# Kernel tuning notes

Hardware: AMD Instinct MI355X
Metric: run time of the kernel (lower is better)

The kernel has to match this reference:

```python
import jax, jax.numpy as jnp
import numpy as np

TEMP = 0.07
MAX_SAMPLES = 2048
RADIUS = 10
HARD_FRAC = 0.75
FG_LABEL = 1
B, C, H, W = 8, 64, 256, 256
BLOCK = 32

MAX_FG = MAX_SAMPLES // 2                      # 1024
NEG_BUDGET = MAX_SAMPLES - MAX_FG              # 1024
HARD_BUDGET = int(round(HARD_FRAC * NEG_BUDGET))  # 768
RAND_BUDGET = NEG_BUDGET - HARD_BUDGET         # 256


def setup_inputs() -> dict:
    key = jax.random.key(0)
    feats = jax.random.normal(key, (B, C, H, W), dtype=jnp.float32)
    # 32x32-block checkerboard labels: guarantees abundant fg / ring / interior-bg pools
    ii, jj = jnp.meshgrid(jnp.arange(H), jnp.arange(W), indexing='ij')
    lbl = (((ii // BLOCK) + (jj // BLOCK)) % 2).astype(jnp.int32)
    labels = jnp.broadcast_to(lbl, (B, H, W))
    return {"feats": feats, "labels": labels}


def _forward(feats, labels):
    Bn, Cn, Hn, Wn = feats.shape
    n_pix = Hn * Wn
    f_flat = feats.reshape(Bn, Cn, n_pix).transpose(0, 2, 1)  # [B, P, C]
    l_flat = labels.reshape(Bn, n_pix)

    fg = labels == FG_LABEL                                   # [B, H, W]
    k = 2 * RADIUS + 1
    # max-pool dilation of fg mask (kernel k, stride 1, pad RADIUS == SAME)
    dil = jax.lax.reduce_window(fg.astype(jnp.float32), -jnp.inf, jax.lax.max,
                                (1, k, k), (1, 1, 1), 'SAME') > 0.0
    fg_flat = fg.reshape(Bn, n_pix)
    bg_flat = ~fg_flat                                        # all pixels valid (no ignore)
    ring_flat = dil.reshape(Bn, n_pix) & ~fg_flat & bg_flat
    bgonly_flat = bg_flat & ~ring_flat

    def per_image(f, y, fgm, ringm, bgm, key):
        k1, k2, k3 = jax.random.split(key, 3)
        def pick(mask, kk, n):
            # random subset of n true positions (== randperm[:n] in distribution)
            s = jnp.where(mask, jax.random.uniform(kk, mask.shape), -1.0)
            return jax.lax.top_k(s, n)[1]
        idx = jnp.concatenate([pick(fgm, k1, MAX_FG),
                               pick(ringm, k2, HARD_BUDGET),
                               pick(bgm, k3, RAND_BUDGET)])    # [K]
        fs = f[idx]                                            # [K, C]
        ys = y[idx]
        fs = fs / jnp.maximum(jnp.linalg.norm(fs, axis=1, keepdims=True), 1e-12)
        logits = fs @ fs.T / TEMP                              # [K, K]
        logits = logits - jax.lax.stop_gradient(logits.max(axis=1, keepdims=True))
        eye = jnp.eye(MAX_SAMPLES, dtype=bool)
        pos = (ys[:, None] == ys[None, :]) & ~eye
        exp_l = jnp.exp(logits) * (~eye)
        denom = jnp.maximum(exp_l.sum(axis=1), 1e-8)
        pos_sum = jnp.maximum(jnp.where(pos, exp_l, 0.0).sum(axis=1), 1e-8)
        valid = pos.any(axis=1) & (ys == FG_LABEL)
        loss_terms = -jnp.log(pos_sum / denom)
        n_valid = jnp.maximum(valid.sum(), 1)
        return jnp.where(valid, loss_terms, 0.0).sum() / n_valid

    keys = jax.random.split(jax.random.key(1), Bn)
    losses = jax.vmap(per_image)(f_flat, l_flat, fg_flat, ring_flat, bgonly_flat, keys)
    return losses.mean()


def reference(feats, labels):
    return _forward(feats, labels)
```

## Files before the change

kernel.cpp:

```cpp
#include <hip/hip_runtime.h>
#include <stdint.h>

#define NPIX   65536
#define NIMG   8
#define NCH    64
#define KSEL   2048
#define NFG    1024
#define NRING  768
#define NBG    256
#define INV_TEMP 14.285714285714286f

__device__ __forceinline__ void tf2x32(uint32_t k0, uint32_t k1,
                                       uint32_t& x0, uint32_t& x1) {
  const uint32_t ks2 = k0 ^ k1 ^ 0x1BD11BDAu;
  x0 += k0; x1 += k1;
#define TF_RND(r) { x0 += x1; x1 = (x1 << (r)) | (x1 >> (32 - (r))); x1 ^= x0; }
  TF_RND(13) TF_RND(15) TF_RND(26) TF_RND(6)
  x0 += k1;  x1 += ks2 + 1u;
  TF_RND(17) TF_RND(29) TF_RND(16) TF_RND(24)
  x0 += ks2; x1 += k0 + 2u;
  TF_RND(13) TF_RND(15) TF_RND(26) TF_RND(6)
  x0 += k0;  x1 += k1 + 3u;
  TF_RND(17) TF_RND(29) TF_RND(16) TF_RND(24)
  x0 += k1;  x1 += ks2 + 4u;
  TF_RND(13) TF_RND(15) TF_RND(26) TF_RND(6)
  x0 += ks2; x1 += k0 + 5u;
#undef TF_RND
}

#define ZERO_F4 1552
__global__ __launch_bounds__(1024) void dilate_pack(const int* __restrict__ labels,
                                                    uint64_t* __restrict__ fgw,
                                                    uint64_t* __restrict__ dilw,
                                                    float4* __restrict__ zregion,
                                                    uint32_t* __restrict__ keys,
                                                    float* __restrict__ out) {
  __shared__ uint64_t fgs[336], hds[336];
  const int tid = threadIdx.x;
  const int img = blockIdx.x >> 2;
  const int r0 = (blockIdx.x & 3) * 64;

  if (blockIdx.x == 0) {
    for (int t = tid; t < ZERO_F4; t += 1024)
      zregion[t] = make_float4(0.f, 0.f, 0.f, 0.f);
  } else if (blockIdx.x == 1 && tid == 0) {
    out[0] = 0.0f;
    for (int b = 0; b < NIMG; ++b) {
      uint32_t kb0 = 0u, kb1 = (uint32_t)b;
      tf2x32(0u, 1u, kb0, kb1);
      for (int g = 0; g < 3; ++g) {
        uint32_t x0 = 0u, x1 = (uint32_t)g;
        tf2x32(kb0, kb1, x0, x1);
        keys[(b * 3 + g) * 2 + 0] = x0;
        keys[(b * 3 + g) * 2 + 1] = x1;
      }
    }
  }

  #pragma unroll
  for (int it = 0; it < 21; ++it) {
    int li = it * 1024 + tid;
    int hr = r0 - 10 + (li >> 8);
    int col = li & 255;
    bool bit = false;
    if (hr >= 0 && hr < 256) bit = (labels[(img << 16) + (hr << 8) + col] == 1);
    uint64_t m = __ballot(bit);
    if ((tid & 63) == 0) fgs[li >> 6] = m;
  }
  __syncthreads();

  for (int w = tid; w < 336; w += 1024) {
    int wc = w & 3;
    uint64_t x = fgs[w];
    uint64_t L = wc > 0 ? fgs[w - 1] : 0ull;
    uint64_t R = wc < 3 ? fgs[w + 1] : 0ull;
    uint64_t acc = x;
    #pragma unroll
    for (int s = 1; s <= 10; ++s) {
      acc |= (x << s) | (L >> (64 - s));
      acc |= (x >> s) | (R << (64 - s));
    }
    hds[w] = acc;
  }
  __syncthreads();

  for (int w = tid; w < 256; w += 1024) {
    int r = w >> 2, wc = w & 3;
    int gr = r0 + r;
    uint64_t acc = 0ull;
    #pragma unroll
    for (int dr = 0; dr <= 20; ++dr) acc |= hds[(r + dr) * 4 + wc];
    fgw[img * 1024 + gr * 4 + wc]  = fgs[(r + 10) * 4 + wc];
    dilw[img * 1024 + gr * 4 + wc] = acc;
  }
}

__global__ __launch_bounds__(256) void hash_hist(const uint64_t* __restrict__ fgw,
                                                 const uint64_t* __restrict__ dilw,
                                                 const uint32_t* __restrict__ keys,
                                                 uint32_t* __restrict__ mgrp,
                                                 uint32_t* __restrict__ hist) {
  __shared__ uint32_t lh[768];
  __shared__ uint64_t fgl[32], dll[32];
  const int tid = threadIdx.x;
  for (int t = tid; t < 768; t += 256) lh[t] = 0;
  const int b = blockIdx.x >> 5;
  const int base = blockIdx.x * 2048;
  const int w0 = (blockIdx.x & 31) * 32;
  if (tid < 32) fgl[tid] = fgw[b * 1024 + w0 + tid];
  else if (tid < 64) dll[tid - 32] = dilw[b * 1024 + w0 + tid - 32];
  const uint32_t K00 = keys[b * 6 + 0], K01 = keys[b * 6 + 1];
  const uint32_t K10 = keys[b * 6 + 2], K11 = keys[b * 6 + 3];
  const uint32_t K20 = keys[b * 6 + 4], K21 = keys[b * 6 + 5];
  __syncthreads();

  #pragma unroll
  for (int k = 0; k < 8; ++k) {
    int off = k * 256 + tid;
    int pix = (base + off) & 65535;
    int lw = off >> 6, bp = off & 63;
    uint32_t fgbit = (uint32_t)((fgl[lw] >> bp) & 1ull);
    uint32_t dilbit = (uint32_t)((dll[lw] >> bp) & 1ull);
    uint32_t grp = fgbit ? 0u : (dilbit ? 1u : 2u);
    uint32_t k0 = grp == 0 ? K00 : grp == 1 ? K10 : K20;
    uint32_t k1 = grp == 0 ? K01 : grp == 1 ? K11 : K21;
    uint32_t x0 = 0u, x1 = (uint32_t)pix;
    tf2x32(k0, k1, x0, x1);
    uint32_t m = (x0 ^ x1) >> 9;
    mgrp[base + off] = (m << 2) | grp;
    atomicAdd(&lh[grp * 256 + (m >> 15)], 1u);
  }
  __syncthreads();
  for (int t = tid; t < 768; t += 256)
    if (lh[t]) atomicAdd(&hist[b * 768 + t], lh[t]);
}

__global__ __launch_bounds__(256) void topk_emit(const uint32_t* __restrict__ mgrp,
                                                 const uint32_t* __restrict__ hist,
                                                 uint32_t* __restrict__ TG,
                                                 uint32_t* __restrict__ cnt,
                                                 uint32_t* __restrict__ candcnt,
                                                 unsigned long long* __restrict__ cand,
                                                 int* __restrict__ idx_out) {
  __shared__ uint32_t hh[768];
  __shared__ uint32_t sT[3], loc[3], lbd[3], basA[3], basB[3];
  const int tid = threadIdx.x;
  const int b = blockIdx.x >> 5;
  const int base = blockIdx.x * 2048;
  for (int t = tid; t < 768; t += 256) hh[t] = hist[b * 768 + t];
  if (tid < 3) { loc[tid] = 0; lbd[tid] = 0; }
  __syncthreads();

  if (tid < 3) {
    uint32_t nsel = tid == 0 ? NFG : tid == 1 ? NRING : NBG;
    const uint32_t* h = hh + tid * 256;
    uint32_t cum = 0; int T = 255;
    for (; T > 0; --T) {
      uint32_t c = h[T];
      if (cum + c >= nsel) break;
      cum += c;
    }
    sT[tid] = (uint32_t)T;
    if ((blockIdx.x & 31) == 0) {
      TG[(b * 3 + tid) * 2] = (uint32_t)T;
      TG[(b * 3 + tid) * 2 + 1] = cum;
    }
  }
  __syncthreads();
  const uint32_t T0 = sT[0], T1 = sT[1], T2 = sT[2];

  #pragma unroll
  for (int k = 0; k < 8; ++k) {
    uint32_t v = mgrp[base + k * 256 + tid];
    uint32_t g = v & 3u, bin = v >> 17;
    uint32_t T = g == 0 ? T0 : g == 1 ? T1 : T2;
    if (bin > T) atomicAdd(&loc[g], 1u);
    else if (bin == T) atomicAdd(&lbd[g], 1u);
  }
  __syncthreads();
  if (tid < 3) {
    basA[tid] = atomicAdd(&cnt[b * 3 + tid], loc[tid]);
    basB[tid] = atomicAdd(&candcnt[b * 3 + tid], lbd[tid]);
    loc[tid] = 0; lbd[tid] = 0;
  }
  __syncthreads();

  #pragma unroll
  for (int k = 0; k < 8; ++k) {
    int p = base + k * 256 + tid;
    uint32_t v = mgrp[p];
    uint32_t g = v & 3u, bin = v >> 17;
    uint32_t T = g == 0 ? T0 : g == 1 ? T1 : T2;
    int pix = p & 65535;
    if (bin > T) {
      uint32_t o = atomicAdd(&loc[g], 1u);
      int seg = g == 0 ? 0 : g == 1 ? NFG : (NFG + NRING);
      idx_out[b * KSEL + seg + (int)(basA[g] + o)] = pix;
    } else if (bin == T) {
      uint32_t o = atomicAdd(&lbd[g], 1u);
      uint32_t c = basB[g] + o;
      uint32_t m = v >> 2;
      if (c < 1024u)
        cand[(b * 3 + g) * 1024 + c] = ((unsigned long long)m << 16) | (uint32_t)pix;
    }
  }
}

#define GA 16
__global__ __launch_bounds__(256) void gather_rank_t(
    const float* __restrict__ feats, const int* __restrict__ idx,
    const uint32_t* __restrict__ TG, const uint32_t* __restrict__ candcnt,
    const unsigned long long* __restrict__ cand, float* __restrict__ fsT) {
  __shared__ float tile[GA * 65];
  __shared__ float ssb[16 * GA];
  __shared__ int lidx[GA];
  __shared__ unsigned long long cb[1024];
  const int tid = threadIdx.x;
  const int img = blockIdx.x >> 7;
  const int win = (blockIdx.x & 127) * GA;
  int seg, segoff, nsel;
  if (win < NFG)               { seg = 0; segoff = 0;            nsel = NFG; }
  else if (win < NFG + NRING)  { seg = 1; segoff = NFG;          nsel = NRING; }
  else                         { seg = 2; segoff = NFG + NRING;  nsel = NBG; }
  const int task = img * 3 + seg;
  const uint32_t G = TG[task * 2 + 1];
  const int poslo = win - segoff;

  if (tid < GA) {
    if ((uint32_t)(poslo + tid) < G)
      lidx[tid] = idx[img * KSEL + win + tid];
  }
  const bool needRank = (uint32_t)(poslo + GA) > G;
  if (needRank) {
    const int c = (int)(candcnt[task] < 1024u ? candcnt[task] : 1024u);
    const int r = nsel - (int)G;
    for (int i = tid; i < c; i += 256) cb[i] = cand[task * 1024 + i];
    __syncthreads();
    for (int i = tid; i < c; i += 256) {
      unsigned long long me = cb[i];
      uint32_t mm = (uint32_t)(me >> 16), pi = (uint32_t)(me & 0xFFFFu);
      int rank = 0;
      for (int j = 0; j < c; ++j) {
        unsigned long long o = cb[j];
        uint32_t om = (uint32_t)(o >> 16), op = (uint32_t)(o & 0xFFFFu);
        if (om > mm || (om == mm && op < pi)) ++rank;
      }
      if (rank < r) {
        int slot = (int)G + rank - poslo;
        if (slot >= 0 && slot < GA) lidx[slot] = (int)pi;
      }
    }
  }
  __syncthreads();

  const int a = tid & 15, q = tid >> 4;
  const int pix = lidx[a];
  const float* fb = feats + ((size_t)img * NCH + q * 4) * NPIX + pix;
  float ss = 0.f;
  #pragma unroll
  for (int k = 0; k < 4; ++k) {
    float v = fb[(size_t)k * NPIX];
    tile[a * 65 + q * 4 + k] = v;
    ss += v * v;
  }
  ssb[q * GA + a] = ss;
  __syncthreads();
  float tot = 0.f;
  #pragma unroll
  for (int q2 = 0; q2 < 16; ++q2) tot += ssb[q2 * GA + a];
  float scale = 1.0f / fmaxf(sqrtf(tot), 1e-12f);
  float* dst = fsT + (size_t)img * NCH * KSEL + win;
  #pragma unroll
  for (int k = 0; k < 4; ++k) {
    int c = q * 4 + k;
    dst[(size_t)c * KSEL + a] = tile[a * 65 + c] * scale;
  }
}

#define LTA 16
__global__ __launch_bounds__(256) void loss_main(const float* __restrict__ fsT,
                                                 float* __restrict__ out) {
  const int img = blockIdx.x & 7;
  const int a0 = (blockIdx.x >> 3) * LTA;
  const float* F = fsT + (size_t)img * NCH * KSEL;
  const float4* F4 = (const float4*)F;
  const int tid = threadIdx.x;

  __shared__ float As[LTA * 64];
  __shared__ float redD[4][LTA], redP[4][LTA], terms[LTA];
  for (int t = tid; t < LTA * 64; t += 256) {
    int a = t & 15, c = t >> 4;
    As[a * 64 + c] = F[(size_t)c * KSEL + a0 + a];
  }
  __syncthreads();

  float acc[LTA][8];
  #pragma unroll
  for (int a = 0; a < LTA; ++a)
    #pragma unroll
    for (int jj = 0; jj < 8; ++jj) acc[a][jj] = 0.f;

  #pragma unroll 2
  for (int c = 0; c < 64; ++c) {
    float4 b0 = F4[c * 512 + tid];
    float4 b1 = F4[c * 512 + 256 + tid];
    #pragma unroll
    for (int a = 0; a < LTA; ++a) {
      float av = As[a * 64 + c];
      acc[a][0] += av * b0.x; acc[a][1] += av * b0.y;
      acc[a][2] += av * b0.z; acc[a][3] += av * b0.w;
      acc[a][4] += av * b1.x; acc[a][5] += av * b1.y;
      acc[a][6] += av * b1.z; acc[a][7] += av * b1.w;
    }
  }

  float pD[LTA], pP[LTA];
  const int jb = 4 * tid;
  #pragma unroll
  for (int a = 0; a < LTA; ++a) {
    const int ag = a0 + a;
    float p = 0.f, d = 0.f;
    #pragma unroll
    for (int jj = 0; jj < 4; ++jj) {
      float e = __expf(acc[a][jj] * INV_TEMP);
      if (jb + jj == ag) e = 0.f;
      p += e;
    }
    #pragma unroll
    for (int jj = 0; jj < 4; ++jj) d += __expf(acc[a][4 + jj] * INV_TEMP);
    pD[a] = d + p;
    pP[a] = p;
  }

  #pragma unroll
  for (int o = 32; o > 0; o >>= 1) {
    #pragma unroll
    for (int a = 0; a < LTA; ++a) {
      pD[a] += __shfl_xor(pD[a], o);
      pP[a] += __shfl_xor(pP[a], o);
    }
  }
  if ((tid & 63) == 0) {
    #pragma unroll
    for (int a = 0; a < LTA; ++a) {
      redD[tid >> 6][a] = pD[a];
      redP[tid >> 6][a] = pP[a];
    }
  }
  __syncthreads();
  if (tid < LTA) {
    float d = redD[0][tid] + redD[1][tid] + redD[2][tid] + redD[3][tid];
    float p = redP[0][tid] + redP[1][tid] + redP[2][tid] + redP[3][tid];
    d = fmaxf(d, 1e-8f); p = fmaxf(p, 1e-8f);
    terms[tid] = __logf(d) - __logf(p);
  }
  __syncthreads();
  if (tid == 0) {
    float s = 0.f;
    #pragma unroll
    for (int a = 0; a < LTA; ++a) s += terms[a];
    atomicAdd(out, s * (1.0f / (NFG * NIMG)));
  }
}

extern "C" void kernel_launch(void* const* d_in, const int* in_sizes, int n_in,
                              void* d_out, int out_size, void* d_ws, size_t ws_size,
                              hipStream_t stream) {
  const float* feats = (const float*)d_in[0];
  const int* labels  = (const int*)d_in[1];
  float* out = (float*)d_out;

  char* ws = (char*)d_ws;
  uint64_t* fgw     = (uint64_t*)(ws);
  uint64_t* dilw    = (uint64_t*)(ws + 65536);
  uint32_t* keys    = (uint32_t*)(ws + 131072);
  uint32_t* TG      = (uint32_t*)(ws + 131328);
  uint32_t* hist    = (uint32_t*)(ws + 131584);
  uint32_t* cnt     = (uint32_t*)(ws + 156160);
  uint32_t* candcnt = (uint32_t*)(ws + 156288);
  unsigned long long* cand = (unsigned long long*)(ws + 156416);
  int*      idx     = (int*)(ws + 353024);
  uint32_t* mgrp    = (uint32_t*)(ws + 524288);
  float*    fsT     = (float*)(ws + 2621440);

  hipLaunchKernelGGL(dilate_pack, dim3(32), dim3(1024), 0, stream,
                     labels, fgw, dilw, (float4*)hist, keys, out);
  hipLaunchKernelGGL(hash_hist, dim3(NIMG * 32), dim3(256), 0, stream,
                     fgw, dilw, keys, mgrp, hist);
  hipLaunchKernelGGL(topk_emit, dim3(NIMG * 32), dim3(256), 0, stream,
                     mgrp, hist, TG, cnt, candcnt, cand, idx);
  hipLaunchKernelGGL(gather_rank_t, dim3((NIMG * KSEL) / GA), dim3(256), 0, stream,
                     feats, idx, TG, candcnt, cand, fsT);
  hipLaunchKernelGGL(loss_main, dim3(NIMG * (NFG / LTA)), dim3(256), 0, stream,
                     fsT, out);
}
```

Before: 250.4 us.

## Compute similarity logits with bf16 MFMA on row-major normalized features

The gather kernel now writes normalized features as bf16 in row-major [K, C] layout instead of fp32 channel-major. The loss kernel is replaced with a matrix-core version that uses 16x16x32 bf16 MFMA instructions to form the 2048x2048 similarity tiles, then does exp, masking and reductions per row. This targets the FP32 FMA cost of the Gram matrix and halves the feature storage traffic. It trades away precision: bf16 inputs to logits that are scaled by 1/0.07 before exp may shift the loss value.

```diff
diff --git a/kernel.cpp b/kernel.cpp
--- a/kernel.cpp
+++ b/kernel.cpp
@@ -9,6 +9,9 @@
 #define NRING  768
 #define NBG    256
 #define INV_TEMP 14.285714285714286f
+
+typedef __attribute__((ext_vector_type(8))) short bf16x8;
+typedef __attribute__((ext_vector_type(4))) float f32x4;
 
 __device__ __forceinline__ void tf2x32(uint32_t k0, uint32_t k1,
                                        uint32_t& x0, uint32_t& x1) {
@@ -28,6 +31,11 @@
 #undef TF_RND
 }
 
+__device__ __forceinline__ ushort f2bf(float f) {
+  uint32_t u = __float_as_uint(f);
+  return (ushort)((u + 0x7FFFu + ((u >> 16) & 1u)) >> 16);
+}
+
 #define ZERO_F4 1552
 __global__ __launch_bounds__(1024) void dilate_pack(const int* __restrict__ labels,
                                                     uint64_t* __restrict__ fgw,
@@ -210,9 +218,10 @@
 __global__ __launch_bounds__(256) void gather_rank_t(
     const float* __restrict__ feats, const int* __restrict__ idx,
     const uint32_t* __restrict__ TG, const uint32_t* __restrict__ candcnt,
-    const unsigned long long* __restrict__ cand, float* __restrict__ fsT) {
+    const unsigned long long* __restrict__ cand, ushort* __restrict__ fs) {
   __shared__ float tile[GA * 65];
   __shared__ float ssb[16 * GA];
+  __shared__ float sscale[GA];
   __shared__ int lidx[GA];
   __shared__ unsigned long long cb[1024];
   const int tid = threadIdx.x;
@@ -265,101 +274,92 @@
   }
   ssb[q * GA + a] = ss;
   __syncthreads();
-  float tot = 0.f;
-  #pragma unroll
-  for (int q2 = 0; q2 < 16; ++q2) tot += ssb[q2 * GA + a];
-  float scale = 1.0f / fmaxf(sqrtf(tot), 1e-12f);
-  float* dst = fsT + (size_t)img * NCH * KSEL + win;
-  #pragma unroll
-  for (int k = 0; k < 4; ++k) {
-    int c = q * 4 + k;
-    dst[(size_t)c * KSEL + a] = tile[a * 65 + c] * scale;
-  }
-}
-
-#define LTA 16
-__global__ __launch_bounds__(256) void loss_main(const float* __restrict__ fsT,
+  if (q == 0) {
+    float tot = 0.f;
+    #pragma unroll
+    for (int q2 = 0; q2 < 16; ++q2) tot += ssb[q2 * GA + a];
+    sscale[a] = 1.0f / fmaxf(sqrtf(tot), 1e-12f);
+  }
+  __syncthreads();
+
+  const int row = tid >> 4, c4 = tid & 15;
+  const float sc = sscale[row];
+  ushort4 v4;
+  v4.x = f2bf(tile[row * 65 + c4 * 4 + 0] * sc);
+  v4.y = f2bf(tile[row * 65 + c4 * 4 + 1] * sc);
+  v4.z = f2bf(tile[row * 65 + c4 * 4 + 2] * sc);
+  v4.w = f2bf(tile[row * 65 + c4 * 4 + 3] * sc);
+  ((ushort4*)(fs + ((size_t)img * KSEL + win + row) * NCH))[c4] = v4;
+}
+
+__global__ __launch_bounds__(256) void loss_mfma(const ushort* __restrict__ fs,
                                                  float* __restrict__ out) {
   const int img = blockIdx.x & 7;
-  const int a0 = (blockIdx.x >> 3) * LTA;
-  const float* F = fsT + (size_t)img * NCH * KSEL;
-  const float4* F4 = (const float4*)F;
-  const int tid = threadIdx.x;
-
-  __shared__ float As[LTA * 64];
-  __shared__ float redD[4][LTA], redP[4][LTA], terms[LTA];
-  for (int t = tid; t < LTA * 64; t += 256) {
-    int a = t & 15, c = t >> 4;
-    As[a * 64 + c] = F[(size_t)c * KSEL + a0 + a];
-  }
-  __syncthreads();
-
-  float acc[LTA][8];
-  #pragma unroll
-  for (int a = 0; a < LTA; ++a)
-    #pragma unroll
-    for (int jj = 0; jj < 8; ++jj) acc[a][jj] = 0.f;
-
-  #pragma unroll 2
-  for (int c = 0; c < 64; ++c) {
-    float4 b0 = F4[c * 512 + tid];
-    float4 b1 = F4[c * 512 + 256 + tid];
-    #pragma unroll
-    for (int a = 0; a < LTA; ++a) {
-      float av = As[a * 64 + c];
-      acc[a][0] += av * b0.x; acc[a][1] += av * b0.y;
-      acc[a][2] += av * b0.z; acc[a][3] += av * b0.w;
-      acc[a][4] += av * b1.x; acc[a][5] += av * b1.y;
-      acc[a][6] += av * b1.z; acc[a][7] += av * b1.w;
-    }
-  }
-
-  float pD[LTA], pP[LTA];
-  const int jb = 4 * tid;
-  #pragma unroll
-  for (int a = 0; a < LTA; ++a) {
-    const int ag = a0 + a;
-    float p = 0.f, d = 0.f;
-    #pragma unroll
-    for (int jj = 0; jj < 4; ++jj) {
-      float e = __expf(acc[a][jj] * INV_TEMP);
-      if (jb + jj == ag) e = 0.f;
-      p += e;
-    }
-    #pragma unroll
-    for (int jj = 0; jj < 4; ++jj) d += __expf(acc[a][4 + jj] * INV_TEMP);
-    pD[a] = d + p;
-    pP[a] = p;
-  }
-
-  #pragma unroll
-  for (int o = 32; o > 0; o >>= 1) {
-    #pragma unroll
-    for (int a = 0; a < LTA; ++a) {
-      pD[a] += __shfl_xor(pD[a], o);
-      pP[a] += __shfl_xor(pP[a], o);
-    }
-  }
-  if ((tid & 63) == 0) {
-    #pragma unroll
-    for (int a = 0; a < LTA; ++a) {
-      redD[tid >> 6][a] = pD[a];
-      redP[tid >> 6][a] = pP[a];
-    }
-  }
-  __syncthreads();
-  if (tid < LTA) {
-    float d = redD[0][tid] + redD[1][tid] + redD[2][tid] + redD[3][tid];
-    float p = redP[0][tid] + redP[1][tid] + redP[2][tid] + redP[3][tid];
-    d = fmaxf(d, 1e-8f); p = fmaxf(p, 1e-8f);
-    terms[tid] = __logf(d) - __logf(p);
-  }
-  __syncthreads();
-  if (tid == 0) {
-    float s = 0.f;
-    #pragma unroll
-    for (int a = 0; a < LTA; ++a) s += terms[a];
-    atomicAdd(out, s * (1.0f / (NFG * NIMG)));
+  const int a0 = (blockIdx.x >> 3) * 32;
+  const ushort* X = fs + (size_t)img * KSEL * NCH;
+  const int tid = threadIdx.x;
+  const int lane = tid & 63, wave = tid >> 6;
+  const int quad = lane >> 4, col = lane & 15;
+  const int rt = wave >> 1, colh = wave & 1;
+
+  __shared__ float redD[2][2][16];
+  __shared__ float redP[2][16];
+
+  const int arow = a0 + rt * 16 + col;
+  const bf16x8* Ap = (const bf16x8*)(X + (size_t)arow * NCH + quad * 8);
+  const bf16x8 a_lo = Ap[0];
+  const bf16x8 a_hi = Ap[4];
+
+  float pD[4] = {0.f, 0.f, 0.f, 0.f};
+  float pP[4] = {0.f, 0.f, 0.f, 0.f};
+  const int ct0 = colh * 64;
+  const int mbase = a0 + rt * 16 + quad * 4;
+
+  for (int ct = ct0; ct < ct0 + 64; ++ct) {
+    const int j = ct * 16 + col;
+    const bf16x8* Bp = (const bf16x8*)(X + (size_t)j * NCH + quad * 8);
+    bf16x8 b_lo = Bp[0];
+    bf16x8 b_hi = Bp[4];
+    f32x4 d = {0.f, 0.f, 0.f, 0.f};
+    d = __builtin_amdgcn_mfma_f32_16x16x32_bf16(a_lo, b_lo, d, 0, 0, 0);
+    d = __builtin_amdgcn_mfma_f32_16x16x32_bf16(a_hi, b_hi, d, 0, 0, 0);
+    #pragma unroll
+    for (int r = 0; r < 4; ++r) {
+      float e = __expf(d[r] * INV_TEMP);
+      if (j == mbase + r) e = 0.f;
+      pD[r] += e;
+      if (colh == 0) pP[r] += e;
+    }
+  }
+
+  #pragma unroll
+  for (int o = 1; o < 16; o <<= 1) {
+    #pragma unroll
+    for (int r = 0; r < 4; ++r) {
+      pD[r] += __shfl_xor(pD[r], o);
+      pP[r] += __shfl_xor(pP[r], o);
+    }
+  }
+  if (col == 0) {
+    #pragma unroll
+    for (int r = 0; r < 4; ++r) {
+      redD[rt][colh][quad * 4 + r] = pD[r];
+      if (colh == 0) redP[rt][quad * 4 + r] = pP[r];
+    }
+  }
+  __syncthreads();
+
+  float term = 0.f;
+  if (tid < 32) {
+    int lrt = tid >> 4, lr = tid & 15;
+    float dsum = fmaxf(redD[lrt][0][lr] + redD[lrt][1][lr], 1e-8f);
+    float psum = fmaxf(redP[lrt][lr], 1e-8f);
+    term = __logf(dsum) - __logf(psum);
+  }
+  if (tid < 64) {
+    #pragma unroll
+    for (int o = 32; o > 0; o >>= 1) term += __shfl_xor(term, o);
+    if (tid == 0) atomicAdd(out, term * (1.0f / (NFG * NIMG)));
   }
 }
 
@@ -381,7 +381,7 @@
   unsigned long long* cand = (unsigned long long*)(ws + 156416);
   int*      idx     = (int*)(ws + 353024);
   uint32_t* mgrp    = (uint32_t*)(ws + 524288);
-  float*    fsT     = (float*)(ws + 2621440);
+  ushort*   fs      = (ushort*)(ws + 2621440);
 
   hipLaunchKernelGGL(dilate_pack, dim3(32), dim3(1024), 0, stream,
                      labels, fgw, dilw, (float4*)hist, keys, out);
@@ -390,7 +390,7 @@
   hipLaunchKernelGGL(topk_emit, dim3(NIMG * 32), dim3(256), 0, stream,
                      mgrp, hist, TG, cnt, candcnt, cand, idx);
   hipLaunchKernelGGL(gather_rank_t, dim3((NIMG * KSEL) / GA), dim3(256), 0, stream,
-                     feats, idx, TG, candcnt, cand, fsT);
-  hipLaunchKernelGGL(loss_main, dim3(NIMG * (NFG / LTA)), dim3(256), 0, stream,
-                     fsT, out);
-}
+                     feats, idx, TG, candcnt, cand, fs);
+  hipLaunchKernelGGL(loss_mfma, dim3(NIMG * (NFG / 32)), dim3(256), 0, stream,
+                     fs, out);
+}
```

Result: faster. 243.9 us (-2.6%).
